# Kernel optimization log

Measured on AMD Instinct MI355X. Metric: run time of the kernel, lower is better.

The kernel has to match this reference:

```python
import jax, jax.numpy as jnp
import numpy as np

B, T, N, DIN, HID, EMB, K, L = 64, 12, 1024, 2, 64, 16, 2, 2


def setup_inputs() -> dict:
    key = jax.random.key(0)
    ks = jax.random.split(key, 10)
    s = lambda i, shape: jax.random.normal(ks[i], shape, dtype=jnp.float32) * 0.1
    return dict(
        x=jax.random.normal(ks[0], (B, T, N, DIN), dtype=jnp.float32),
        init_state=jnp.zeros((L, B, N, HID), dtype=jnp.float32),
        node_embed=s(1, (N, EMB)),
        gw0=s(2, (EMB, K, DIN + HID, 2 * HID)), gb0=s(3, (EMB, 2 * HID)),
        uw0=s(4, (EMB, K, DIN + HID, HID)), ub0=s(5, (EMB, HID)),
        gw1=s(6, (EMB, K, HID + HID, 2 * HID)), gb1=s(7, (EMB, 2 * HID)),
        uw1=s(8, (EMB, K, HID + HID, HID)), ub1=s(9, (EMB, HID)),
    )


def _supports(E):
    # adaptive adjacency: softmax(relu(E E^T)) and Chebyshev set [I, A, 2A*T_{k-1}-T_{k-2}]
    A = jax.nn.softmax(jax.nn.relu(E @ E.T), axis=1)
    sup = [jnp.eye(E.shape[0], dtype=E.dtype), A]
    for _ in range(2, K):
        sup.append(2.0 * A @ sup[-1] - sup[-2])
    return jnp.stack(sup, 0)  # [K, N, N]


def _gconv(inp, supports, W, b):
    # inp: [B,N,Ci]; original does 'knm,bmc->bknc' then permute to bnkc -> fused here
    xg = jnp.einsum('knm,bmc->bnkc', supports, inp)
    return jnp.einsum('bnki,nkio->bno', xg, W) + b


def _layer(x_seq, state0, supports, Wg, bg, Wu, bu):
    def step(state, x_t):
        zr = jax.nn.sigmoid(_gconv(jnp.concatenate([x_t, state], -1), supports, Wg, bg))
        z, r = zr[..., :HID], zr[..., HID:]
        hc = jnp.tanh(_gconv(jnp.concatenate([x_t, z * state], -1), supports, Wu, bu))
        h = r * state + (1.0 - r) * hc
        return h, h

    xs = jnp.swapaxes(x_seq, 0, 1)  # [T,B,N,C]
    last, hs = jax.lax.scan(step, state0, xs)
    return jnp.swapaxes(hs, 0, 1), last  # [B,T,N,HID], [B,N,HID]


def reference(x, init_state, node_embed, gw0, gb0, uw0, ub0, gw1, gb1, uw1, ub1):
    sup = _supports(node_embed)
    mkW = lambda wp: jnp.einsum('nd,dkio->nkio', node_embed, wp)  # per-node weights
    mkb = lambda bp: node_embed @ bp  # per-node bias
    cur = x
    lasts = []
    for i, (gw, gb, uw, ub) in enumerate([(gw0, gb0, uw0, ub0), (gw1, gb1, uw1, ub1)]):
        cur, last = _layer(cur, init_state[i], sup, mkW(gw), mkb(gb), mkW(uw), mkb(ub))
        lasts.append(last)
    return cur, jnp.stack(lasts, 0)
```

## Files before the change

kernel.cpp:

```cpp
#include <hip/hip_runtime.h>
#include <cmath>

constexpr int kN = 1024;
constexpr int kB = 64;
constexpr int kT = 12;
constexpr int kH = 64;
constexpr int kE = 16;
constexpr long long OUT0 = (long long)kB * kT * kN * kH;
constexpr long long BNH = (long long)kB * kN * kH;

typedef __attribute__((ext_vector_type(8))) __bf16 bf16x8;
typedef __attribute__((ext_vector_type(4))) float f32x4;
typedef unsigned short u16;

struct StepPtrs {
  const u16* s0;
  const u16* s1;
  const u16* zr;
  const float* x;
  const u16* ax;
  const u16* d1;
  const u16* d2;
  const u16* d3;
};

__device__ __forceinline__ float sig_(float v) { return 1.f / (1.f + expf(-v)); }

__device__ __forceinline__ u16 f2bf(float f) {
  unsigned u = __float_as_uint(f);
  unsigned r = u + 0x7FFFu + ((u >> 16) & 1u);
  return (u16)(r >> 16);
}
__device__ __forceinline__ float bf2f(u16 s) {
  return __uint_as_float(((unsigned)s) << 16);
}

__device__ __forceinline__ void gload16(const void* g, void* l) {
  __builtin_amdgcn_global_load_lds((const __attribute__((address_space(1))) void*)g,
                                   (__attribute__((address_space(3))) void*)l, 16, 0, 0);
}

__device__ __forceinline__ ushort4 mulbf4(ushort4 a, ushort4 b) {
  ushort4 r;
  r.x = f2bf(bf2f(a.x) * bf2f(b.x));
  r.y = f2bf(bf2f(a.y) * bf2f(b.y));
  r.z = f2bf(bf2f(a.z) * bf2f(b.z));
  r.w = f2bf(bf2f(a.w) * bf2f(b.w));
  return r;
}

__global__ void __launch_bounds__(256) cvt_state(const float* __restrict__ in,
                                                 u16* __restrict__ out) {
  int i = (blockIdx.x * 256 + threadIdx.x) * 4;
  float4 v = *(const float4*)&in[i];
  ushort4 h;
  h.x = f2bf(v.x); h.y = f2bf(v.y); h.z = f2bf(v.z); h.w = f2bf(v.w);
  *(ushort4*)&out[i] = h;
}

__global__ void __launch_bounds__(256) compute_A(const float* __restrict__ E,
                                                 u16* __restrict__ Ah) {
  int n = blockIdx.x, tx = threadIdx.x;
  __shared__ float En[kE];
  __shared__ float red[4];
  if (tx < kE) En[tx] = E[n * kE + tx];
  __syncthreads();
  float v[4];
  float mx = 0.f;
#pragma unroll
  for (int i = 0; i < 4; ++i) {
    int m = tx + i * 256;
    float s = 0.f;
#pragma unroll
    for (int d = 0; d < kE; ++d) s += En[d] * E[m * kE + d];
    s = fmaxf(s, 0.f);
    v[i] = s;
    mx = fmaxf(mx, s);
  }
#pragma unroll
  for (int off = 32; off; off >>= 1) mx = fmaxf(mx, __shfl_down(mx, off));
  int wid = tx >> 6, lane = tx & 63;
  if (lane == 0) red[wid] = mx;
  __syncthreads();
  mx = fmaxf(fmaxf(red[0], red[1]), fmaxf(red[2], red[3]));
  __syncthreads();
  float sum = 0.f;
#pragma unroll
  for (int i = 0; i < 4; ++i) {
    v[i] = expf(v[i] - mx);
    sum += v[i];
  }
#pragma unroll
  for (int off = 32; off; off >>= 1) sum += __shfl_down(sum, off);
  if (lane == 0) red[wid] = sum;
  __syncthreads();
  sum = red[0] + red[1] + red[2] + red[3];
  float inv = 1.f / sum;
#pragma unroll
  for (int i = 0; i < 4; ++i) {
    int m = tx + i * 256;
    Ah[n * kN + m] = f2bf(v[i] * inv);
  }
}

__global__ void __launch_bounds__(256) mkw2(const float* __restrict__ E,
                                            const float* __restrict__ Wsrc,
                                            u16* __restrict__ Wh,
                                            int O, int KI, int KIp, int Idim, int mode) {
  int o = blockIdx.x;
  int n0 = blockIdx.y * 128;
  int ki = threadIdx.x;
  __shared__ float Es[128][kE + 1];
  for (int idx = threadIdx.x; idx < 128 * kE; idx += 256)
    Es[idx >> 4][idx & 15] = E[(n0 + (idx >> 4)) * kE + (idx & 15)];
  __syncthreads();
  if (ki >= KIp) return;
  float w[kE];
  if (ki < KI) {
    int k, i;
    if (mode == 0) {
      k = ki >> 7;
      i = ki & 127;
    } else {
      if (ki < 128) {
        k = ki >> 6;
        i = (ki & 63) + 2;
      } else {
        k = (ki - 128) >> 1;
        i = (ki - 128) & 1;
      }
    }
#pragma unroll
    for (int d = 0; d < kE; ++d) w[d] = Wsrc[((d * 2 + k) * Idim + i) * O + o];
  } else {
#pragma unroll
    for (int d = 0; d < kE; ++d) w[d] = 0.f;
  }
  int NKT = KIp >> 5;
  int kt = ki >> 5, qq = (ki >> 3) & 3, j = ki & 7;
  for (int nn = 0; nn < 128; ++nn) {
    float acc = 0.f;
#pragma unroll
    for (int d = 0; d < kE; ++d) acc += Es[nn][d] * w[d];
    Wh[((((long long)(n0 + nn) * NKT + kt) * 4 + qq) * O + o) * 8 + j] = f2bf(acc);
  }
}

__global__ void __launch_bounds__(256) mkb(const float* __restrict__ E,
                                           const float* __restrict__ bsrc,
                                           float* __restrict__ out, int O) {
  int idx = blockIdx.x * 256 + threadIdx.x;
  int n = idx / O, o = idx - n * O;
  if (n >= kN) return;
  float acc = 0.f;
#pragma unroll
  for (int d = 0; d < kE; ++d) acc += E[n * kE + d] * bsrc[d * O + o];
  out[idx] = acc;
}

__global__ void __launch_bounds__(256) prep_x(const float* __restrict__ x,
                                              u16* __restrict__ Vth) {
  int m0 = blockIdx.x * 64, bt0 = blockIdx.y * 32, tid = threadIdx.x;
  __shared__ u16 T[64][68];
  for (int idx = tid; idx < 2048; idx += 256) {
    int mi = idx & 63, j = idx >> 6;
    float2 v = *(const float2*)&x[((long long)(bt0 + j) * kN + m0 + mi) * 2];
    T[j * 2 + 0][mi] = f2bf(v.x);
    T[j * 2 + 1][mi] = f2bf(v.y);
  }
  __syncthreads();
  for (int idx = tid; idx < 1024; idx += 256) {
    int cc = idx >> 4, mi4 = (idx & 15) * 4;
    ushort4 v = *(const ushort4*)&T[cc][mi4];
    *(ushort4*)&Vth[(long long)(bt0 * 2 + cc) * kN + m0 + mi4] = v;
  }
}

__global__ void __launch_bounds__(256) prep_split(const u16* __restrict__ srcA,
                                                  const u16* __restrict__ srcB,
                                                  const u16* __restrict__ mul,
                                                  u16* __restrict__ Vth) {
  int b = blockIdx.y, m0 = blockIdx.x * 64, tid = threadIdx.x;
  int z = blockIdx.z;
  const u16* src = z ? srcB : srcA;
  int colBase = z * 4096;
  __shared__ u16 T[64][68];
  for (int idx = tid; idx < 1024; idx += 256) {
    int mi = idx >> 4, c4 = (idx & 15) * 4;
    long long rowi = (long long)b * kN + m0 + mi;
    ushort4 v = *(const ushort4*)&src[rowi * 64 + c4];
    if (mul) {
      ushort4 mz = *(const ushort4*)&mul[rowi * 128 + c4];
      v = mulbf4(v, mz);
    }
    T[c4 + 0][mi] = v.x;
    T[c4 + 1][mi] = v.y;
    T[c4 + 2][mi] = v.z;
    T[c4 + 3][mi] = v.w;
  }
  __syncthreads();
  for (int idx = tid; idx < 1024; idx += 256) {
    int c = idx >> 4, mi4 = (idx & 15) * 4;
    ushort4 v = *(const ushort4*)&T[c][mi4];
    *(ushort4*)&Vth[(long long)(colBase + b * 64 + c) * kN + m0 + mi4] = v;
  }
}

__global__ void __launch_bounds__(512, 4) diff_gemm(const u16* __restrict__ Ah,
                                                    const u16* __restrict__ Vth,
                                                    u16* __restrict__ outp, int sh) {
  __shared__ __align__(16) u16 lds[2][8192];
  int tid = threadIdx.x;
  int lane = tid & 63;
  int q = lane >> 4, r16 = lane & 15;
  int wave = tid >> 6;
  int wm = wave >> 2, wn = wave & 3;
  int m0 = blockIdx.y * 128, n0 = blockIdx.x * 128;

  const u16* gsrc[2];
  int ldst[2];
#pragma unroll
  for (int j = 0; j < 2; ++j) {
    int ci = j * 512 + tid;
    int tile = ci >> 9, idx = ci & 511;
    int row = idx >> 2, sp = idx & 3;
    int sl = sp ^ ((row >> 1) & 3);
    const u16* s = tile ? Vth : Ah;
    int gr = (tile ? n0 : m0) + row;
    gsrc[j] = s + (long long)gr * kN + sl * 8;
    ldst[j] = ci * 8;
  }
  int aoff[4], voff[2];
#pragma unroll
  for (int fm = 0; fm < 4; ++fm) {
    int row = wm * 64 + fm * 16 + r16;
    aoff[fm] = row * 32 + (q ^ ((row >> 1) & 3)) * 8;
  }
#pragma unroll
  for (int fn = 0; fn < 2; ++fn) {
    int col = wn * 32 + fn * 16 + r16;
    voff[fn] = 4096 + col * 32 + (q ^ ((col >> 1) & 3)) * 8;
  }
  f32x4 acc[4][2];
#pragma unroll
  for (int fm = 0; fm < 4; ++fm)
#pragma unroll
    for (int fn = 0; fn < 2; ++fn) acc[fm][fn] = (f32x4){0.f, 0.f, 0.f, 0.f};

  auto STAGE = [&](int buf, int kt) {
#pragma unroll
    for (int j = 0; j < 2; ++j) gload16(gsrc[j] + kt * 32, &lds[buf][ldst[j]]);
  };
  auto COMPUTE = [&](int buf) {
    const u16* L = &lds[buf][0];
    bf16x8 ah[4], vh[2];
#pragma unroll
    for (int fm = 0; fm < 4; ++fm) ah[fm] = *(const bf16x8*)&L[aoff[fm]];
#pragma unroll
    for (int fn = 0; fn < 2; ++fn) vh[fn] = *(const bf16x8*)&L[voff[fn]];
#pragma unroll
    for (int fm = 0; fm < 4; ++fm)
#pragma unroll
      for (int fn = 0; fn < 2; ++fn)
        acc[fm][fn] =
            __builtin_amdgcn_mfma_f32_16x16x32_bf16(ah[fm], vh[fn], acc[fm][fn], 0, 0, 0);
  };

  STAGE(0, 0);
  asm volatile("s_waitcnt vmcnt(0)" ::: "memory");
  __builtin_amdgcn_s_barrier();
#pragma unroll 1
  for (int kt = 0; kt < 30; kt += 2) {
    STAGE(1, kt + 1);
    COMPUTE(0);
    asm volatile("s_waitcnt vmcnt(0)" ::: "memory");
    __builtin_amdgcn_s_barrier();
    STAGE(0, kt + 2);
    COMPUTE(1);
    asm volatile("s_waitcnt vmcnt(0)" ::: "memory");
    __builtin_amdgcn_s_barrier();
  }
  STAGE(1, 31);
  COMPUTE(0);
  asm volatile("s_waitcnt vmcnt(0)" ::: "memory");
  __builtin_amdgcn_s_barrier();
  COMPUTE(1);

  int msk = (1 << sh) - 1;
#pragma unroll
  for (int fm = 0; fm < 4; ++fm)
#pragma unroll
    for (int fn = 0; fn < 2; ++fn) {
      int nrow = m0 + wm * 64 + fm * 16 + q * 4;
      int col = n0 + wn * 32 + fn * 16 + r16;
      long long b = col >> sh;
      int c = col & msk;
#pragma unroll
      for (int r = 0; r < 4; ++r)
        outp[(((b * kN + nrow + r)) << sh) + c] = f2bf(acc[fm][fn][r]);
    }
}

template <int VAR, int O, int KIp>
__global__ void __launch_bounds__(256, 2) mfma_node(StepPtrs P,
                                                    const u16* __restrict__ Wh,
                                                    const float* __restrict__ bias,
                                                    u16* __restrict__ zr_out,
                                                    u16* __restrict__ state_out,
                                                    float* __restrict__ seq_out,
                                                    float* __restrict__ last_out, int t) {
  constexpr int S = KIp + 8;
  constexpr int NKT = KIp / 32;
  constexpr int NF = (O == 128) ? 2 : 1;
  __shared__ __align__(16) u16 Xs[64 * S];
  int n = blockIdx.x;
  int tid = threadIdx.x;
  int lane = tid & 63, wave = tid >> 6;
  int q = lane >> 4, r16 = lane & 15;
  int colbase = (O == 128) ? wave * 32 : wave * 16;

  bf16x8 wreg[NKT][NF];
#pragma unroll
  for (int kt = 0; kt < NKT; ++kt)
#pragma unroll
    for (int fn = 0; fn < NF; ++fn)
      wreg[kt][fn] = *(const bf16x8*)&Wh[((((long long)n * NKT + kt) * 4 + q) * O +
                                          colbase + fn * 16 + r16) * 8];

  if constexpr (VAR == 0 || VAR == 1) {
    for (int idx = tid; idx < 1024; idx += 256) {
      int b = idx >> 4, c4 = (idx & 15) << 2;
      long long bn = (long long)b * kN + n;
      ushort4 v0 = *(const ushort4*)&P.s0[bn * 64 + c4];
      if (VAR == 1) {
        ushort4 z = *(const ushort4*)&P.zr[bn * 128 + c4];
        v0 = mulbf4(v0, z);
      }
      *(ushort4*)&Xs[b * S + c4] = v0;
      ushort4 v1 = *(const ushort4*)&P.d1[bn * 64 + c4];
      *(ushort4*)&Xs[b * S + 64 + c4] = v1;
    }
    if (tid < 128) {
      int b = tid >> 1, c = tid & 1;
      long long btn = ((long long)b * kT + t) * kN + n;
      Xs[b * S + 128 + c] = f2bf(P.x[btn * 2 + c]);
      Xs[b * S + 130 + c] = P.ax[btn * 2 + c];
    }
    for (int idx = tid; idx < 448; idx += 256) {
      int b = idx / 7, c = 132 + (idx % 7) * 4;
      ushort4 zz = {0, 0, 0, 0};
      *(ushort4*)&Xs[b * S + c] = zz;
    }
  } else {
    for (int idx = tid; idx < 1024; idx += 256) {
      int b = idx >> 4, c4 = (idx & 15) << 2;
      long long bn = (long long)b * kN + n;
      ushort4 v0 = *(const ushort4*)&P.s0[bn * 64 + c4];
      *(ushort4*)&Xs[b * S + c4] = v0;
      ushort4 v1 = *(const ushort4*)&P.s1[bn * 64 + c4];
      if (VAR == 3) {
        ushort4 z = *(const ushort4*)&P.zr[bn * 128 + c4];
        v1 = mulbf4(v1, z);
      }
      *(ushort4*)&Xs[b * S + 64 + c4] = v1;
      ushort4 v2 = *(const ushort4*)&P.d2[bn * 64 + c4];
      *(ushort4*)&Xs[b * S + 128 + c4] = v2;
      ushort4 v3 = *(const ushort4*)&P.d3[bn * 64 + c4];
      *(ushort4*)&Xs[b * S + 192 + c4] = v3;
    }
  }
  __syncthreads();

  f32x4 acc[4][NF];
#pragma unroll
  for (int fm = 0; fm < 4; ++fm)
#pragma unroll
    for (int fn = 0; fn < NF; ++fn) acc[fm][fn] = (f32x4){0.f, 0.f, 0.f, 0.f};

#pragma unroll
  for (int kt = 0; kt < NKT; ++kt) {
    int kb = kt * 32 + q * 8;
    bf16x8 xh[4];
#pragma unroll
    for (int fm = 0; fm < 4; ++fm)
      xh[fm] = *(const bf16x8*)&Xs[(fm * 16 + r16) * S + kb];
#pragma unroll
    for (int fm = 0; fm < 4; ++fm)
#pragma unroll
      for (int fn = 0; fn < NF; ++fn)
        acc[fm][fn] =
            __builtin_amdgcn_mfma_f32_16x16x32_bf16(xh[fm], wreg[kt][fn], acc[fm][fn], 0, 0, 0);
  }

  if constexpr (O == 128) {
#pragma unroll
    for (int fn = 0; fn < NF; ++fn) {
      int o = colbase + fn * 16 + r16;
      float bb = bias[n * 128 + o];
#pragma unroll
      for (int fm = 0; fm < 4; ++fm) {
#pragma unroll
        for (int r = 0; r < 4; ++r) {
          int b = fm * 16 + q * 4 + r;
          zr_out[((long long)b * kN + n) * 128 + o] = f2bf(sig_(acc[fm][fn][r] + bb));
        }
      }
    }
  } else {
    const u16* sptr = (VAR == 1) ? P.s0 : P.s1;
    int o = colbase + r16;
    float bb = bias[n * 64 + o];
#pragma unroll
    for (int fm = 0; fm < 4; ++fm) {
#pragma unroll
      for (int r = 0; r < 4; ++r) {
        int b = fm * 16 + q * 4 + r;
        long long bn = (long long)b * kN + n;
        float rr = bf2f(P.zr[bn * 128 + 64 + o]);
        float sv = bf2f(sptr[bn * 64 + o]);
        float h = rr * sv + (1.f - rr) * tanhf(acc[fm][0][r] + bb);
        state_out[bn * 64 + o] = f2bf(h);
        if constexpr (VAR == 3) {
          seq_out[(((long long)b * kT + t) * kN + n) * 64 + o] = h;
        }
        if (t == kT - 1) last_out[bn * 64 + o] = h;
      }
    }
  }
}

extern "C" void kernel_launch(void* const* d_in, const int* in_sizes, int n_in, void* d_out,
                              int out_size, void* d_ws, size_t ws_size, hipStream_t stream) {
  (void)in_sizes; (void)n_in; (void)out_size; (void)ws_size;
  const float* x   = (const float*)d_in[0];
  const float* ist = (const float*)d_in[1];
  const float* E   = (const float*)d_in[2];
  const float* gw0 = (const float*)d_in[3];
  const float* gb0 = (const float*)d_in[4];
  const float* uw0 = (const float*)d_in[5];
  const float* ub0 = (const float*)d_in[6];
  const float* gw1 = (const float*)d_in[7];
  const float* gb1 = (const float*)d_in[8];
  const float* uw1 = (const float*)d_in[9];
  const float* ub1 = (const float*)d_in[10];
  float* out = (float*)d_out;

  char* base = (char*)d_ws;
  size_t off = 0;
  auto alloc = [&](size_t bytes) {
    char* p = base + off;
    off += (bytes + 1023) & ~(size_t)1023;
    return p;
  };
  u16* Vth = (u16*)alloc((size_t)8192 * kN * 2);
  u16* Ahh = (u16*)alloc((size_t)kN * kN * 2);
  u16* Ax = (u16*)alloc((size_t)kB * kT * kN * 2 * 2);
  u16* Wg0h = (u16*)alloc((size_t)kN * 128 * 160 * 2);
  u16* Wu0h = (u16*)alloc((size_t)kN * 64 * 160 * 2);
  u16* Wg1h = (u16*)alloc((size_t)kN * 128 * 256 * 2);
  u16* Wu1h = (u16*)alloc((size_t)kN * 64 * 256 * 2);
  float* Bg0 = (float*)alloc((size_t)kN * 128 * 4);
  float* Bu0 = (float*)alloc((size_t)kN * 64 * 4);
  float* Bg1 = (float*)alloc((size_t)kN * 128 * 4);
  float* Bu1 = (float*)alloc((size_t)kN * 64 * 4);
  u16* ss = (u16*)alloc((size_t)BNH * 2 * 2);
  u16* dx = (u16*)alloc((size_t)BNH * 2);
  u16* dd = (u16*)alloc((size_t)BNH * 2 * 2);
  u16* zr = (u16*)alloc((size_t)kB * kN * 128 * 2);
  u16* s0 = ss;
  u16* s1 = ss + BNH;
  u16* d2 = dd;
  u16* d3 = dd + BNH;

  cvt_state<<<(int)(2 * BNH / 1024), 256, 0, stream>>>(ist, ss);

  compute_A<<<kN, 256, 0, stream>>>(E, Ahh);
  prep_x<<<dim3(16, 24), 256, 0, stream>>>(x, Vth);
  diff_gemm<<<dim3(12, 8), 512, 0, stream>>>(Ahh, Vth, Ax, 1);

  mkw2<<<dim3(128, 8), 256, 0, stream>>>(E, gw0, Wg0h, 128, 132, 160, 66, 1);
  mkw2<<<dim3(64, 8), 256, 0, stream>>>(E, uw0, Wu0h, 64, 132, 160, 66, 1);
  mkw2<<<dim3(128, 8), 256, 0, stream>>>(E, gw1, Wg1h, 128, 256, 256, 128, 0);
  mkw2<<<dim3(64, 8), 256, 0, stream>>>(E, uw1, Wu1h, 64, 256, 256, 128, 0);
  mkb<<<(kN * 128) / 256, 256, 0, stream>>>(E, gb0, Bg0, 128);
  mkb<<<(kN * 64) / 256, 256, 0, stream>>>(E, ub0, Bu0, 64);
  mkb<<<(kN * 128) / 256, 256, 0, stream>>>(E, gb1, Bg1, 128);
  mkb<<<(kN * 64) / 256, 256, 0, stream>>>(E, ub1, Bu1, 64);

  prep_split<<<dim3(16, kB, 1), 256, 0, stream>>>(s0, nullptr, nullptr, Vth);
  diff_gemm<<<dim3(32, 8), 512, 0, stream>>>(Ahh, Vth, d2, 6);

  for (int t = 0; t < kT; ++t) {
    StepPtrs Pg0{s0, s1, zr, x, Ax, d2, d2, d3};
    mfma_node<0, 128, 160><<<kN, 256, 0, stream>>>(Pg0, Wg0h, Bg0, zr, nullptr,
                                                   nullptr, nullptr, t);
    prep_split<<<dim3(16, kB, 1), 256, 0, stream>>>(s0, nullptr, zr, Vth);
    diff_gemm<<<dim3(32, 8), 512, 0, stream>>>(Ahh, Vth, dx, 6);
    StepPtrs Pu0{s0, s1, zr, x, Ax, dx, d2, d3};
    mfma_node<1, 64, 160><<<kN, 256, 0, stream>>>(Pu0, Wu0h, Bu0, nullptr, s0,
                                                  nullptr, out + OUT0, t);
    prep_split<<<dim3(16, kB, 2), 256, 0, stream>>>(s0, s1, nullptr, Vth);
    diff_gemm<<<dim3(64, 8), 512, 0, stream>>>(Ahh, Vth, d2, 6);
    StepPtrs P1g{s0, s1, zr, x, Ax, d2, d2, d3};
    mfma_node<2, 128, 256><<<kN, 256, 0, stream>>>(P1g, Wg1h, Bg1, zr, nullptr,
                                                   nullptr, nullptr, t);
    prep_split<<<dim3(16, kB, 1), 256, 0, stream>>>(s1, nullptr, zr, Vth);
    diff_gemm<<<dim3(32, 8), 512, 0, stream>>>(Ahh, Vth, dx, 6);
    StepPtrs P1u{s0, s1, zr, x, Ax, d2, d2, dx};
    mfma_node<3, 64, 256><<<kN, 256, 0, stream>>>(P1u, Wu1h, Bu1, nullptr, s1, out,
                                                  out + OUT0 + BNH, t);
  }
}
```

Baseline: 2.166 ms.

## Add wider-tile diffusion GEMM for layer-1 gate and simplify per-node weight layout

Adds diff_gemm2, a 128x256 output-tile variant of the diffusion GEMM with a 4x4 MFMA fragment grid per wave. It is used for the layer-1 gate diffusion step, which covers two state tensors, so half as many blocks are launched and each loaded A tile is reused across more columns. Separately, the per-node bf16 weight layout changes from a fragment-interleaved order to plain [n][o][KI], with the node kernel's load indexing updated to match. The wider tile raises register and LDS pressure per block, and the new weight layout may change how well the weight loads coalesce.

```diff
diff --git a/kernel.cpp b/kernel.cpp
--- a/kernel.cpp
+++ b/kernel.cpp
@@ -136,13 +136,11 @@
 #pragma unroll
     for (int d = 0; d < kE; ++d) w[d] = 0.f;
   }
-  int NKT = KIp >> 5;
-  int kt = ki >> 5, qq = (ki >> 3) & 3, j = ki & 7;
   for (int nn = 0; nn < 128; ++nn) {
     float acc = 0.f;
 #pragma unroll
     for (int d = 0; d < kE; ++d) acc += Es[nn][d] * w[d];
-    Wh[((((long long)(n0 + nn) * NKT + kt) * 4 + qq) * O + o) * 8 + j] = f2bf(acc);
+    Wh[((long long)(n0 + nn) * O + o) * KIp + ki] = f2bf(acc);
   }
 }
 
@@ -298,6 +296,101 @@
 #pragma unroll
       for (int r = 0; r < 4; ++r)
         outp[(((b * kN + nrow + r)) << sh) + c] = f2bf(acc[fm][fn][r]);
+    }
+}
+
+__global__ void __launch_bounds__(512, 2) diff_gemm2(const u16* __restrict__ Ah,
+                                                     const u16* __restrict__ Vth,
+                                                     u16* __restrict__ outp) {
+  __shared__ __align__(16) u16 lds[2][24576];
+  int tid = threadIdx.x;
+  int lane = tid & 63;
+  int q = lane >> 4, r16 = lane & 15;
+  int wave = tid >> 6;
+  int wm = wave >> 2, wn = wave & 3;
+  int m0 = blockIdx.y * 128, n0 = blockIdx.x * 256;
+
+  const u16* gsrc[3];
+  int ldst[3];
+  {
+    int row = tid >> 2, sp = tid & 3;
+    gsrc[0] = Ah + (long long)(m0 + row) * kN + (sp ^ ((row >> 1) & 3)) * 8;
+    ldst[0] = tid * 8;
+  }
+#pragma unroll
+  for (int j = 1; j < 3; ++j) {
+    int vi = (j - 1) * 512 + tid;
+    int row = vi >> 2, sp = vi & 3;
+    gsrc[j] = Vth + (long long)(n0 + row) * kN + (sp ^ ((row >> 1) & 3)) * 8;
+    ldst[j] = 8192 + vi * 8;
+  }
+  int aoff[4], voff[4];
+#pragma unroll
+  for (int fm = 0; fm < 4; ++fm) {
+    int row = wm * 64 + fm * 16 + r16;
+    aoff[fm] = row * 32 + (q ^ ((row >> 1) & 3)) * 8;
+  }
+#pragma unroll
+  for (int fn = 0; fn < 4; ++fn) {
+    int col = wn * 64 + fn * 16 + r16;
+    voff[fn] = 8192 + col * 32 + (q ^ ((col >> 1) & 3)) * 8;
+  }
+  f32x4 acc[4][4];
+#pragma unroll
+  for (int fm = 0; fm < 4; ++fm)
+#pragma unroll
+    for (int fn = 0; fn < 4; ++fn) acc[fm][fn] = (f32x4){0.f, 0.f, 0.f, 0.f};
+
+  auto STAGE = [&](int buf, int kt) {
+#pragma unroll
+    for (int j = 0; j < 3; ++j) gload16(gsrc[j] + kt * 32, &lds[buf][ldst[j]]);
+  };
+  auto COMPUTE = [&](int buf) {
+    const u16* L = &lds[buf][0];
+    bf16x8 ah[4], vh[4];
+#pragma unroll
+    for (int fm = 0; fm < 4; ++fm) ah[fm] = *(const bf16x8*)&L[aoff[fm]];
+#pragma unroll
+    for (int fn = 0; fn < 4; ++fn) vh[fn] = *(const bf16x8*)&L[voff[fn]];
+#pragma unroll
+    for (int fm = 0; fm < 4; ++fm)
+#pragma unroll
+      for (int fn = 0; fn < 4; ++fn)
+        acc[fm][fn] =
+            __builtin_amdgcn_mfma_f32_16x16x32_bf16(ah[fm], vh[fn], acc[fm][fn], 0, 0, 0);
+  };
+
+  STAGE(0, 0);
+  asm volatile("s_waitcnt vmcnt(0)" ::: "memory");
+  __builtin_amdgcn_s_barrier();
+#pragma unroll 1
+  for (int kt = 0; kt < 30; kt += 2) {
+    STAGE(1, kt + 1);
+    COMPUTE(0);
+    asm volatile("s_waitcnt vmcnt(0)" ::: "memory");
+    __builtin_amdgcn_s_barrier();
+    STAGE(0, kt + 2);
+    COMPUTE(1);
+    asm volatile("s_waitcnt vmcnt(0)" ::: "memory");
+    __builtin_amdgcn_s_barrier();
+  }
+  STAGE(1, 31);
+  COMPUTE(0);
+  asm volatile("s_waitcnt vmcnt(0)" ::: "memory");
+  __builtin_amdgcn_s_barrier();
+  COMPUTE(1);
+
+#pragma unroll
+  for (int fm = 0; fm < 4; ++fm)
+#pragma unroll
+    for (int fn = 0; fn < 4; ++fn) {
+      int nrow = m0 + wm * 64 + fm * 16 + q * 4;
+      int col = n0 + wn * 64 + fn * 16 + r16;
+      long long b = col >> 6;
+      int c = col & 63;
+#pragma unroll
+      for (int r = 0; r < 4; ++r)
+        outp[((b * kN + nrow + r) << 6) + c] = f2bf(acc[fm][fn][r]);
     }
 }
 
@@ -324,8 +417,8 @@
   for (int kt = 0; kt < NKT; ++kt)
 #pragma unroll
     for (int fn = 0; fn < NF; ++fn)
-      wreg[kt][fn] = *(const bf16x8*)&Wh[((((long long)n * NKT + kt) * 4 + q) * O +
-                                          colbase + fn * 16 + r16) * 8];
+      wreg[kt][fn] = *(const bf16x8*)&Wh[((long long)n * O + colbase + fn * 16 + r16) * KIp +
+                                         kt * 32 + q * 8];
 
   if constexpr (VAR == 0 || VAR == 1) {
     for (int idx = tid; idx < 1024; idx += 256) {
@@ -500,7 +593,7 @@
     mfma_node<1, 64, 160><<<kN, 256, 0, stream>>>(Pu0, Wu0h, Bu0, nullptr, s0,
                                                   nullptr, out + OUT0, t);
     prep_split<<<dim3(16, kB, 2), 256, 0, stream>>>(s0, s1, nullptr, Vth);
-    diff_gemm<<<dim3(64, 8), 512, 0, stream>>>(Ahh, Vth, d2, 6);
+    diff_gemm2<<<dim3(32, 8), 512, 0, stream>>>(Ahh, Vth, d2);
     StepPtrs P1g{s0, s1, zr, x, Ax, d2, d2, d3};
     mfma_node<2, 128, 256><<<kN, 256, 0, stream>>>(P1g, Wg1h, Bg1, zr, nullptr,
                                                    nullptr, nullptr, t);
```

New measurement: 2.192 ms. Within noise of the previous version (+1.2%).

## Wavefront-pipeline the two GRU layers and fuse paired gate/update launches

Applied to the files above, without the earlier changes.

Restructures the time loop so layer 0 at step t+1 runs alongside layer 1 at step t. Paired gate and update kernels launch 2N blocks each, and the diffusion GEMMs for both layers are batched into wider launches. The goal is fewer serialized launches and fuller GPU occupancy, at the cost of double-buffered state and zr buffers and more complex indexing. The per-node weight layout also changes from an MFMA-tiled format to a plain row-major [n][o][ki] layout, which may make the weight register loads less coalesced.

```diff
diff --git a/kernel.cpp b/kernel.cpp
--- a/kernel.cpp
+++ b/kernel.cpp
@@ -136,13 +136,11 @@
 #pragma unroll
     for (int d = 0; d < kE; ++d) w[d] = 0.f;
   }
-  int NKT = KIp >> 5;
-  int kt = ki >> 5, qq = (ki >> 3) & 3, j = ki & 7;
   for (int nn = 0; nn < 128; ++nn) {
     float acc = 0.f;
 #pragma unroll
     for (int d = 0; d < kE; ++d) acc += Es[nn][d] * w[d];
-    Wh[((((long long)(n0 + nn) * NKT + kt) * 4 + qq) * O + o) * 8 + j] = f2bf(acc);
+    Wh[((long long)(n0 + nn) * O + o) * KIp + ki] = f2bf(acc);
   }
 }
 
@@ -178,11 +176,13 @@
 
 __global__ void __launch_bounds__(256) prep_split(const u16* __restrict__ srcA,
                                                   const u16* __restrict__ srcB,
-                                                  const u16* __restrict__ mul,
+                                                  const u16* __restrict__ mulA,
+                                                  const u16* __restrict__ mulB,
                                                   u16* __restrict__ Vth) {
   int b = blockIdx.y, m0 = blockIdx.x * 64, tid = threadIdx.x;
   int z = blockIdx.z;
   const u16* src = z ? srcB : srcA;
+  const u16* mul = z ? mulB : mulA;
   int colBase = z * 4096;
   __shared__ u16 T[64][68];
   for (int idx = tid; idx < 1024; idx += 256) {
@@ -302,18 +302,17 @@
 }
 
 template <int VAR, int O, int KIp>
-__global__ void __launch_bounds__(256, 2) mfma_node(StepPtrs P,
-                                                    const u16* __restrict__ Wh,
-                                                    const float* __restrict__ bias,
-                                                    u16* __restrict__ zr_out,
-                                                    u16* __restrict__ state_out,
-                                                    float* __restrict__ seq_out,
-                                                    float* __restrict__ last_out, int t) {
+__device__ __forceinline__ void mfma_body(int n, const StepPtrs& P,
+                                          const u16* __restrict__ Wh,
+                                          const float* __restrict__ bias,
+                                          u16* __restrict__ zr_out,
+                                          u16* __restrict__ state_out,
+                                          float* __restrict__ seq_out,
+                                          float* __restrict__ last_out, int t) {
   constexpr int S = KIp + 8;
   constexpr int NKT = KIp / 32;
   constexpr int NF = (O == 128) ? 2 : 1;
-  __shared__ __align__(16) u16 Xs[64 * S];
-  int n = blockIdx.x;
+  __shared__ __align__(16) u16 Xs[64 * (256 + 8)];
   int tid = threadIdx.x;
   int lane = tid & 63, wave = tid >> 6;
   int q = lane >> 4, r16 = lane & 15;
@@ -324,8 +323,8 @@
   for (int kt = 0; kt < NKT; ++kt)
 #pragma unroll
     for (int fn = 0; fn < NF; ++fn)
-      wreg[kt][fn] = *(const bf16x8*)&Wh[((((long long)n * NKT + kt) * 4 + q) * O +
-                                          colbase + fn * 16 + r16) * 8];
+      wreg[kt][fn] = *(const bf16x8*)&Wh[((long long)n * O + colbase + fn * 16 + r16) * KIp +
+                                         kt * 32 + q * 8];
 
   if constexpr (VAR == 0 || VAR == 1) {
     for (int idx = tid; idx < 1024; idx += 256) {
@@ -427,6 +426,43 @@
       }
     }
   }
+}
+
+template <int VAR, int O, int KIp>
+__global__ void __launch_bounds__(256, 2) mfma_node(StepPtrs P, const u16* __restrict__ Wh,
+                                                    const float* __restrict__ bias,
+                                                    u16* __restrict__ zr_out,
+                                                    u16* __restrict__ state_out,
+                                                    float* __restrict__ seq_out,
+                                                    float* __restrict__ last_out, int t) {
+  mfma_body<VAR, O, KIp>(blockIdx.x, P, Wh, bias, zr_out, state_out, seq_out, last_out, t);
+}
+
+__global__ void __launch_bounds__(256, 2) gate_pair(StepPtrs Pa, const u16* __restrict__ Wa,
+                                                    const float* __restrict__ Ba,
+                                                    u16* __restrict__ zra,
+                                                    StepPtrs Pb, const u16* __restrict__ Wb,
+                                                    const float* __restrict__ Bb,
+                                                    u16* __restrict__ zrb, int tb) {
+  if (blockIdx.x < kN)
+    mfma_body<2, 128, 256>(blockIdx.x, Pa, Wa, Ba, zra, nullptr, nullptr, nullptr, 0);
+  else
+    mfma_body<0, 128, 160>(blockIdx.x - kN, Pb, Wb, Bb, zrb, nullptr, nullptr, nullptr, tb);
+}
+
+__global__ void __launch_bounds__(256, 2) update_pair(StepPtrs Pa, const u16* __restrict__ Wa,
+                                                      const float* __restrict__ Ba,
+                                                      u16* __restrict__ s1out,
+                                                      float* __restrict__ seq,
+                                                      float* __restrict__ lastA, int ta,
+                                                      StepPtrs Pb, const u16* __restrict__ Wb,
+                                                      const float* __restrict__ Bb,
+                                                      u16* __restrict__ s0out,
+                                                      float* __restrict__ lastB, int tb) {
+  if (blockIdx.x < kN)
+    mfma_body<3, 64, 256>(blockIdx.x, Pa, Wa, Ba, nullptr, s1out, seq, lastA, ta);
+  else
+    mfma_body<1, 64, 160>(blockIdx.x - kN, Pb, Wb, Bb, nullptr, s0out, nullptr, lastB, tb);
 }
 
 extern "C" void kernel_launch(void* const* d_in, const int* in_sizes, int n_in, void* d_out,
@@ -463,16 +499,20 @@
   float* Bu0 = (float*)alloc((size_t)kN * 64 * 4);
   float* Bg1 = (float*)alloc((size_t)kN * 128 * 4);
   float* Bu1 = (float*)alloc((size_t)kN * 64 * 4);
-  u16* ss = (u16*)alloc((size_t)BNH * 2 * 2);
-  u16* dx = (u16*)alloc((size_t)BNH * 2);
+  u16* ssA = (u16*)alloc((size_t)BNH * 2 * 2);
+  u16* s0B = (u16*)alloc((size_t)BNH * 2);
+  u16* ddx = (u16*)alloc((size_t)BNH * 2 * 2);
   u16* dd = (u16*)alloc((size_t)BNH * 2 * 2);
-  u16* zr = (u16*)alloc((size_t)kB * kN * 128 * 2);
-  u16* s0 = ss;
-  u16* s1 = ss + BNH;
+  u16* zr0 = (u16*)alloc((size_t)kB * kN * 128 * 2);
+  u16* zr1 = (u16*)alloc((size_t)kB * kN * 128 * 2);
+  u16* s0buf[2] = {ssA, s0B};
+  u16* s1 = ssA + BNH;
+  u16* dxA = ddx;
+  u16* dxB = ddx + BNH;
   u16* d2 = dd;
   u16* d3 = dd + BNH;
 
-  cvt_state<<<(int)(2 * BNH / 1024), 256, 0, stream>>>(ist, ss);
+  cvt_state<<<(int)(2 * BNH / 1024), 256, 0, stream>>>(ist, ssA);
 
   compute_A<<<kN, 256, 0, stream>>>(E, Ahh);
   prep_x<<<dim3(16, 24), 256, 0, stream>>>(x, Vth);
@@ -487,27 +527,50 @@
   mkb<<<(kN * 128) / 256, 256, 0, stream>>>(E, gb1, Bg1, 128);
   mkb<<<(kN * 64) / 256, 256, 0, stream>>>(E, ub1, Bu1, 64);
 
-  prep_split<<<dim3(16, kB, 1), 256, 0, stream>>>(s0, nullptr, nullptr, Vth);
+  prep_split<<<dim3(16, kB, 1), 256, 0, stream>>>(s0buf[0], nullptr, nullptr, nullptr, Vth);
   diff_gemm<<<dim3(32, 8), 512, 0, stream>>>(Ahh, Vth, d2, 6);
 
+  {
+    StepPtrs Pg0{s0buf[0], s1, zr0, x, Ax, d2, d2, d3};
+    mfma_node<0, 128, 160><<<kN, 256, 0, stream>>>(Pg0, Wg0h, Bg0, zr0, nullptr, nullptr,
+                                                   nullptr, 0);
+    prep_split<<<dim3(16, kB, 1), 256, 0, stream>>>(s0buf[0], nullptr, zr0, nullptr, Vth);
+    diff_gemm<<<dim3(32, 8), 512, 0, stream>>>(Ahh, Vth, dxB, 6);
+  }
+
   for (int t = 0; t < kT; ++t) {
-    StepPtrs Pg0{s0, s1, zr, x, Ax, d2, d2, d3};
-    mfma_node<0, 128, 160><<<kN, 256, 0, stream>>>(Pg0, Wg0h, Bg0, zr, nullptr,
-                                                   nullptr, nullptr, t);
-    prep_split<<<dim3(16, kB, 1), 256, 0, stream>>>(s0, nullptr, zr, Vth);
-    diff_gemm<<<dim3(32, 8), 512, 0, stream>>>(Ahh, Vth, dx, 6);
-    StepPtrs Pu0{s0, s1, zr, x, Ax, dx, d2, d3};
-    mfma_node<1, 64, 160><<<kN, 256, 0, stream>>>(Pu0, Wu0h, Bu0, nullptr, s0,
-                                                  nullptr, out + OUT0, t);
-    prep_split<<<dim3(16, kB, 2), 256, 0, stream>>>(s0, s1, nullptr, Vth);
-    diff_gemm<<<dim3(64, 8), 512, 0, stream>>>(Ahh, Vth, d2, 6);
-    StepPtrs P1g{s0, s1, zr, x, Ax, d2, d2, d3};
-    mfma_node<2, 128, 256><<<kN, 256, 0, stream>>>(P1g, Wg1h, Bg1, zr, nullptr,
-                                                   nullptr, nullptr, t);
-    prep_split<<<dim3(16, kB, 1), 256, 0, stream>>>(s1, nullptr, zr, Vth);
-    diff_gemm<<<dim3(32, 8), 512, 0, stream>>>(Ahh, Vth, dx, 6);
-    StepPtrs P1u{s0, s1, zr, x, Ax, d2, d2, dx};
-    mfma_node<3, 64, 256><<<kN, 256, 0, stream>>>(P1u, Wu1h, Bu1, nullptr, s1, out,
-                                                  out + OUT0 + BNH, t);
-  }
-}
+    u16* sCur = s0buf[t & 1];
+    u16* sNxt = s0buf[(t + 1) & 1];
+    StepPtrs P1{sCur, s1, zr0, x, Ax, dxB, d2, d3};
+    if (t == 0) {
+      mfma_node<1, 64, 160><<<kN, 256, 0, stream>>>(P1, Wu0h, Bu0, nullptr, sNxt, nullptr,
+                                                    out + OUT0, 0);
+    } else {
+      StepPtrs P3{sCur, s1, zr1, x, Ax, dxA, d2, dxA};
+      update_pair<<<2 * kN, 256, 0, stream>>>(P3, Wu1h, Bu1, s1, out, out + OUT0 + BNH, t - 1,
+                                              P1, Wu0h, Bu0, sNxt, out + OUT0, t);
+    }
+    prep_split<<<dim3(16, kB, 2), 256, 0, stream>>>(sNxt, s1, nullptr, nullptr, Vth);
+    diff_gemm<<<dim3(64, 8), 512, 0, stream>>>(Ahh, Vth, dd, 6);
+    StepPtrs P2{sNxt, s1, zr1, x, Ax, d2, d2, d3};
+    if (t < kT - 1) {
+      StepPtrs P0{sNxt, s1, zr0, x, Ax, d2, d2, d3};
+      gate_pair<<<2 * kN, 256, 0, stream>>>(P2, Wg1h, Bg1, zr1, P0, Wg0h, Bg0, zr0, t + 1);
+    } else {
+      mfma_node<2, 128, 256><<<kN, 256, 0, stream>>>(P2, Wg1h, Bg1, zr1, nullptr, nullptr,
+                                                     nullptr, 0);
+    }
+    if (t < kT - 1) {
+      prep_split<<<dim3(16, kB, 2), 256, 0, stream>>>(s1, sNxt, zr1, zr0, Vth);
+      diff_gemm<<<dim3(64, 8), 512, 0, stream>>>(Ahh, Vth, ddx, 6);
+    } else {
+      prep_split<<<dim3(16, kB, 1), 256, 0, stream>>>(s1, nullptr, zr1, nullptr, Vth);
+      diff_gemm<<<dim3(32, 8), 512, 0, stream>>>(Ahh, Vth, dxA, 6);
+    }
+  }
+  {
+    StepPtrs P3{s0buf[0], s1, zr1, x, Ax, dxA, d2, dxA};
+    mfma_node<3, 64, 256><<<kN, 256, 0, stream>>>(P3, Wu1h, Bu1, nullptr, s1, out,
+                                                  out + OUT0 + BNH, kT - 1);
+  }
+}
```

New measurement: 2.124 ms. No clear change (-1.9%).
